# Kernel tuning notes

Hardware: AMD Instinct MI355X
Metric: run time of the kernel (lower is better)

## Reference

```python
import jax, jax.numpy as jnp
import numpy as np

HIDDEN = 2048
N_HEADS = 16
HEAD_DIM = HIDDEN // N_HEADS
ROPE_BASE = 10000.0


def rotate_half(x):
    half = x.shape[-1] // 2
    return jnp.concatenate((-x[..., half:], x[..., :half]), axis=-1)


def rope_cos_sin(seq_len, dtype):
    inv_freq = 1.0 / (ROPE_BASE ** (jnp.arange(0, HEAD_DIM, 2, dtype=jnp.float32) / HEAD_DIM))
    pos = jnp.arange(seq_len, dtype=jnp.float32)
    freqs = jnp.einsum('i,j->ij', pos, inv_freq)  # [S, hd/2]
    emb = jnp.concatenate((freqs, freqs), axis=-1)  # [S, hd]
    return jnp.cos(emb).astype(dtype), jnp.sin(emb).astype(dtype)


def setup_inputs() -> dict:
    key = jax.random.key(0)
    ks = jax.random.split(key, 9)
    B, S, H = 2, 2048, HIDDEN
    std = 1.0 / np.sqrt(H)
    return {
        'hidden_states': jax.random.normal(ks[0], (B, S, H), dtype=jnp.float32),
        'Wq': jax.random.uniform(ks[1], (H, H), jnp.float32, -std, std),
        'bq': jax.random.uniform(ks[2], (H,), jnp.float32, -std, std),
        'Wk': jax.random.uniform(ks[3], (H, H), jnp.float32, -std, std),
        'bk': jax.random.uniform(ks[4], (H,), jnp.float32, -std, std),
        'Wv': jax.random.uniform(ks[5], (H, H), jnp.float32, -std, std),
        'bv': jax.random.uniform(ks[6], (H,), jnp.float32, -std, std),
        'Wo': jax.random.uniform(ks[7], (H, H), jnp.float32, -std, std),
        'bo': jax.random.uniform(ks[8], (H,), jnp.float32, -std, std),
    }


def reference(hidden_states, Wq, bq, Wk, bk, Wv, bv, Wo, bo):
    B, S, H = hidden_states.shape
    scale = HEAD_DIM ** -0.5

    def proj(W, b):
        # torch Linear: x @ W.T + b
        y = jnp.einsum('bsh,oh->bso', hidden_states, W) + b
        return y.reshape(B, S, N_HEADS, HEAD_DIM).transpose(0, 2, 1, 3)  # [B,nh,S,hd]

    q = proj(Wq, bq)
    k = proj(Wk, bk)
    v = proj(Wv, bv)

    cos, sin = rope_cos_sin(S, hidden_states.dtype)  # [S, hd]
    cos = cos[None, None, :, :]
    sin = sin[None, None, :, :]
    q = q * cos + rotate_half(q) * sin
    k = k * cos + rotate_half(k) * sin

    scores = jnp.einsum('bhqd,bhkd->bhqk', q, k) * scale  # [B,nh,S,S]
    probs = jax.nn.softmax(scores, axis=-1)
    ctx = jnp.einsum('bhqk,bhkd->bhqd', probs, v)
    ctx = ctx.transpose(0, 2, 1, 3).reshape(B, S, H)
    return jnp.einsum('bsh,oh->bso', ctx, Wo) + bo
```

## Files before the change

kernel.cpp:

```cpp
#include <hip/hip_runtime.h>
#include <hip/hip_bf16.h>
#include <math.h>

#define HIDDEN 2048
#define NH 16
#define HD 128
#define NB 2
#define SEQ 2048
#define K_DIM 2048

typedef unsigned int u32;
typedef unsigned short ushort_t;
typedef __bf16 bf16x8 __attribute__((ext_vector_type(8)));
typedef float f32x4 __attribute__((ext_vector_type(4)));
typedef ushort_t u16x8 __attribute__((ext_vector_type(8)));

__device__ __forceinline__ void split1(float x, unsigned short& h, unsigned short& l) {
    u32 u = __float_as_uint(x);
    u32 hr = (u + 0x7FFFu + ((u >> 16) & 1u)) >> 16;
    h = (unsigned short)hr;
    float r = x - __uint_as_float(hr << 16);
    u32 u2 = __float_as_uint(r);
    l = (unsigned short)((u2 + 0x7FFFu + ((u2 >> 16) & 1u)) >> 16);
}

__device__ __forceinline__ ushort_t bf16r(float x) {
    u32 u = __float_as_uint(x);
    return (ushort_t)((u + 0x7FFFu + ((u >> 16) & 1u)) >> 16);
}

__device__ __forceinline__ void gl_lds16(const void* g, void* l) {
    __builtin_amdgcn_global_load_lds(
        (const __attribute__((address_space(1))) u32*)g,
        (__attribute__((address_space(3))) u32*)l, 16, 0, 0);
}

__global__ void k_rope_tables(float* __restrict__ ct, float* __restrict__ st) {
    int idx = blockIdx.x * 256 + threadIdx.x;
    int s = idx >> 6, d = idx & 63;
    double inv = pow(10000.0, -(double)d * (1.0 / 64.0));
    double ang = (double)s * inv;
    ct[idx] = (float)cos(ang);
    st[idx] = (float)sin(ang);
}

#define XG 2097152
#define WG 1048576
__global__ void k_cvt_all(const float4* __restrict__ X, const float4* __restrict__ W0,
                          const float4* __restrict__ W1, const float4* __restrict__ W2,
                          ushort4* __restrict__ Xh, ushort4* __restrict__ H0,
                          ushort4* __restrict__ H1, ushort4* __restrict__ H2) {
    int idx = blockIdx.x * 256 + threadIdx.x;
    const float4* src;
    ushort4* dst;
    int off;
    if (idx < XG) { src = X; dst = Xh; off = idx; }
    else {
        int t = idx - XG;
        int m = t >> 20;
        off = t & (WG - 1);
        src = (m == 0) ? W0 : (m == 1) ? W1 : W2;
        dst = (m == 0) ? H0 : (m == 1) ? H1 : H2;
    }
    float4 x = src[off];
    ushort4 h;
    h.x = bf16r(x.x); h.y = bf16r(x.y); h.z = bf16r(x.z); h.w = bf16r(x.w);
    dst[off] = h;
}

__global__ void k_split(const float4* __restrict__ src, ushort4* __restrict__ hi,
                        ushort4* __restrict__ lo) {
    int idx = blockIdx.x * 256 + threadIdx.x;
    float4 x = src[idx];
    ushort4 h, l;
    split1(x.x, h.x, l.x);
    split1(x.y, h.y, l.y);
    split1(x.z, h.z, l.z);
    split1(x.w, h.w, l.w);
    hi[idx] = h;
    lo[idx] = l;
}

#define BAR  __builtin_amdgcn_s_barrier()
#define VM8  asm volatile("s_waitcnt vmcnt(8)" ::: "memory")
#define VM0  asm volatile("s_waitcnt vmcnt(0)" ::: "memory")
#define PRIO1 __builtin_amdgcn_s_setprio(1)
#define PRIO0 __builtin_amdgcn_s_setprio(0)

#define STA(slot, half, kt) do { \
    const ushort_t* g_ = Xh + sgA + (size_t)((half) * 128) * 2048 + (size_t)(kt) * 64; \
    gl_lds16(g_, &As[slot][((half) * 128 + w * 16) * 64]); \
    gl_lds16(g_ + 8 * 2048, &As[slot][((half) * 128 + w * 16 + 8) * 64]); \
} while (0)

#define STB(slot, half, kt) do { \
    const ushort_t* g_ = Wsel + sgB + (size_t)((half) * 128) * 2048 + (size_t)(kt) * 64; \
    gl_lds16(g_, &Bs[slot][((half) * 128 + w * 16) * 64]); \
    gl_lds16(g_ + 8 * 2048, &Bs[slot][((half) * 128 + w * 16 + 8) * 64]); \
} while (0)

#define STAGE_T(slot, kt) do { \
    STA(slot, 0, kt); STA(slot, 1, kt); STB(slot, 0, kt); STB(slot, 1, kt); \
} while (0)

#define RD_A4(DST, slot, MB) \
    _Pragma("unroll") for (int mf = 0; mf < 4; mf++) { \
        DST[mf][0] = *(const bf16x8*)&As[slot][arow + ((MB) + mf) * 1024 + cc0]; \
        DST[mf][1] = *(const bf16x8*)&As[slot][arow + ((MB) + mf) * 1024 + cc1]; \
    }

#define RD_B2(DST, slot, NBB) \
    _Pragma("unroll") for (int nf = 0; nf < 2; nf++) { \
        DST[nf][0] = *(const bf16x8*)&Bs[slot][brow + ((NBB) + nf) * 1024 + cc0]; \
        DST[nf][1] = *(const bf16x8*)&Bs[slot][brow + ((NBB) + nf) * 1024 + cc1]; \
    }

#define PH_MFMA(AF, BF, MB, NBB) do { PRIO1; \
    _Pragma("unroll") for (int mf = 0; mf < 4; mf++) \
    _Pragma("unroll") for (int nf = 0; nf < 2; nf++) { \
        acc[(MB) + mf][(NBB) + nf] = __builtin_amdgcn_mfma_f32_16x16x32_bf16( \
            AF[mf][0], BF[nf][0], acc[(MB) + mf][(NBB) + nf], 0, 0, 0); \
        acc[(MB) + mf][(NBB) + nf] = __builtin_amdgcn_mfma_f32_16x16x32_bf16( \
            AF[mf][1], BF[nf][1], acc[(MB) + mf][(NBB) + nf], 0, 0, 0); \
    } PRIO0; } while (0)

#define KTILE(slot) do { \
    RD_A4(a03, slot, 0); RD_B2(b01, slot, 0); \
    RD_A4(a47, slot, 4); RD_B2(b23, slot, 2); \
    PH_MFMA(a03, b01, 0, 0); \
    PH_MFMA(a47, b01, 4, 0); \
    PH_MFMA(a03, b23, 0, 2); \
    PH_MFMA(a47, b23, 4, 2); \
} while (0)

__global__ __launch_bounds__(512, 2)
void k_gemm_qkv8(const ushort_t* __restrict__ Xh,
                 const ushort_t* __restrict__ W0, const ushort_t* __restrict__ W1,
                 const ushort_t* __restrict__ W2,
                 const float* __restrict__ b0, const float* __restrict__ b1,
                 const float* __restrict__ b2,
                 float* __restrict__ o0, float* __restrict__ o1, float* __restrict__ o2) {
    __shared__ ushort_t As[2][256 * 64];
    __shared__ ushort_t Bs[2][256 * 64];
    const int tid = threadIdx.x;
    const int lane = tid & 63;
    const int w = tid >> 6;
    const int wm = w >> 2;
    const int wn = w & 3;
    const int quad = lane >> 4;
    const int l15 = lane & 15;

    int bid = blockIdx.x;
    bid = (bid & 7) * 48 + (bid >> 3);
    const int bx = bid & 15;
    const int by = bid >> 4;
    const int m0 = bx << 8;
    const int mat = by >> 3;
    const int n0 = (by & 7) << 8;
    const ushort_t* Wsel = (mat == 0) ? W0 : (mat == 1) ? W1 : W2;
    const float* bias = (mat == 0) ? b0 : (mat == 1) ? b1 : b2;
    float* out = (mat == 0) ? o0 : (mat == 1) ? o1 : o2;

    const int lrow = lane >> 3;
    const int lcol8 = (((lane & 7) ^ lrow) << 3);
    const size_t sgA = (size_t)(m0 + w * 16 + lrow) * 2048 + lcol8;
    const size_t sgB = (size_t)(n0 + w * 16 + lrow) * 2048 + lcol8;

    const int arow = (wm * 128 + l15) * 64;
    const int brow = (wn * 64 + l15) * 64;
    const int cc0 = ((quad ^ (l15 & 7)) << 3);
    const int cc1 = cc0 ^ 32;

    f32x4 acc[8][4];
#pragma unroll
    for (int i = 0; i < 8; i++)
#pragma unroll
        for (int j = 0; j < 4; j++) acc[i][j] = (f32x4){0.f, 0.f, 0.f, 0.f};

    bf16x8 a03[4][2], a47[4][2], b01[2][2], b23[2][2];

    STAGE_T(0, 0);

    for (int it = 0; it < 16; ++it) {
        STAGE_T(1, 2 * it + 1);
        VM8;
        BAR;
        KTILE(0);
        BAR;
        if (it < 15) { STAGE_T(0, 2 * it + 2); VM8; } else { VM0; }
        BAR;
        KTILE(1);
        BAR;
    }

    float bcolv[4];
#pragma unroll
    for (int nf = 0; nf < 4; nf++) bcolv[nf] = bias[n0 + wn * 64 + nf * 16 + l15];

    const int mbase = m0 + wm * 128 + quad * 4;
#pragma unroll
    for (int mf = 0; mf < 8; mf++)
#pragma unroll
        for (int nf = 0; nf < 4; nf++) {
            const int n = n0 + wn * 64 + nf * 16 + l15;
            const int hh = n >> 7;
            const int d = n & 127;
#pragma unroll
            for (int r = 0; r < 4; r++) {
                const int m = mbase + mf * 16 + r;
                const int bb = m >> 11;
                const int s = m & (SEQ - 1);
                out[((size_t)(bb * NH + hh) * SEQ + s) * HD + d] = acc[mf][nf][r] + bcolv[nf];
            }
        }
}

__global__ __launch_bounds__(256)
void k_gemm_o(const ushort_t* __restrict__ Ah, const ushort_t* __restrict__ Al,
              const ushort_t* __restrict__ Bh, const ushort_t* __restrict__ Bl,
              const float* __restrict__ bias, float* __restrict__ out) {
    __shared__ ushort_t lds[4][128 * 32];
    const int tid = threadIdx.x;
    const int lane = tid & 63;
    const int w = tid >> 6;
    const int wm = w & 1, wn = w >> 1;
    const int quad = lane >> 4;
    const int l15 = lane & 15;
    const int m0 = blockIdx.x << 7;
    const int n0 = blockIdx.y << 7;
    const bool isA = (w < 2);

    const ushort_t* src = (w == 0) ? Ah : (w == 1) ? Al : (w == 2) ? Bh : Bl;
    const int lrow = lane >> 2;
    const int lk = (lane & 3) << 3;
    const ushort_t* gp[8];
    ushort_t* lp[8];
#pragma unroll
    for (int i = 0; i < 8; i++) {
        if (isA) {
            int m = m0 + i * 16 + lrow;
            int bb = m >> 11, s = m & (SEQ - 1);
            gp[i] = src + ((size_t)bb * NH * SEQ + s) * HD + lk;
        } else {
            gp[i] = src + (size_t)(n0 + i * 16 + lrow) * K_DIM + lk;
        }
        lp[i] = &lds[w][i * 512];
    }

    f32x4 acc[4][4];
#pragma unroll
    for (int i = 0; i < 4; i++)
#pragma unroll
        for (int j = 0; j < 4; j++) acc[i][j] = (f32x4){0.f, 0.f, 0.f, 0.f};

    const int aoff = (wm * 64 + l15) * 32 + quad * 8;
    const int boff = (wn * 64 + l15) * 32 + quad * 8;

#pragma unroll
    for (int i = 0; i < 8; i++) gl_lds16(gp[i], lp[i]);
    __syncthreads();
    bf16x8 ah[4], al[4], bh[4], bl[4];
#pragma unroll
    for (int f = 0; f < 4; f++) {
        ah[f] = *(const bf16x8*)&lds[0][aoff + f * 512];
        al[f] = *(const bf16x8*)&lds[1][aoff + f * 512];
        bh[f] = *(const bf16x8*)&lds[2][boff + f * 512];
        bl[f] = *(const bf16x8*)&lds[3][boff + f * 512];
    }

    for (int kt = 32; kt <= K_DIM; kt += 32) {
        __syncthreads();
        if (kt < K_DIM) {
            const size_t koff = isA ? ((size_t)(kt >> 7) * (SEQ * HD) + (kt & 127)) : (size_t)kt;
#pragma unroll
            for (int i = 0; i < 8; i++) gl_lds16(gp[i] + koff, lp[i]);
        }
#pragma unroll
        for (int fm = 0; fm < 4; fm++)
#pragma unroll
            for (int fn = 0; fn < 4; fn++) {
                acc[fm][fn] = __builtin_amdgcn_mfma_f32_16x16x32_bf16(ah[fm], bh[fn], acc[fm][fn], 0, 0, 0);
                acc[fm][fn] = __builtin_amdgcn_mfma_f32_16x16x32_bf16(ah[fm], bl[fn], acc[fm][fn], 0, 0, 0);
                acc[fm][fn] = __builtin_amdgcn_mfma_f32_16x16x32_bf16(al[fm], bh[fn], acc[fm][fn], 0, 0, 0);
            }
        if (kt < K_DIM) {
            __syncthreads();
#pragma unroll
            for (int f = 0; f < 4; f++) {
                ah[f] = *(const bf16x8*)&lds[0][aoff + f * 512];
                al[f] = *(const bf16x8*)&lds[1][aoff + f * 512];
                bh[f] = *(const bf16x8*)&lds[2][boff + f * 512];
                bl[f] = *(const bf16x8*)&lds[3][boff + f * 512];
            }
        }
    }

    float bcolv[4];
#pragma unroll
    for (int fn = 0; fn < 4; fn++) bcolv[fn] = bias[n0 + wn * 64 + fn * 16 + l15];

    const int mb = m0 + wm * 64 + quad * 4;
    const int nb = n0 + wn * 64 + l15;
#pragma unroll
    for (int fm = 0; fm < 4; fm++)
#pragma unroll
        for (int fn = 0; fn < 4; fn++)
#pragma unroll
            for (int r = 0; r < 4; r++)
                out[(size_t)(mb + fm * 16 + r) * HIDDEN + nb + fn * 16] =
                    acc[fm][fn][r] + bcolv[fn];
}

__global__ void k_rope_pack(const float* __restrict__ q, const float* __restrict__ k,
                            const float* __restrict__ ct, const float* __restrict__ st,
                            ushort_t* __restrict__ Qb, ushort_t* __restrict__ Kb) {
    int idx = blockIdx.x * 256 + threadIdx.x;
    int d = idx & 63;
    int s = (idx >> 6) & (SEQ - 1);
    int bh = idx >> 17;
    size_t base = ((size_t)bh * SEQ + s) * HD;
    float c = ct[(s << 6) + d], sn = st[(s << 6) + d];
    const float scq = 0.08838834764831845f;
    float q0 = q[base + d], q1 = q[base + d + 64];
    Qb[base + d]      = bf16r((q0 * c - q1 * sn) * scq);
    Qb[base + d + 64] = bf16r((q1 * c + q0 * sn) * scq);
    float k0 = k[base + d], k1 = k[base + d + 64];
    Kb[base + d]      = bf16r(k0 * c - k1 * sn);
    Kb[base + d + 64] = bf16r(k1 * c + k0 * sn);
}

__global__ __launch_bounds__(256)
void k_vpack(const float* __restrict__ v, ushort_t* __restrict__ vt) {
    __shared__ float t[64][65];
    const int tid = threadIdx.x;
    const int bh = blockIdx.z;
    const int s0 = blockIdx.x << 6;
    const int d0 = blockIdx.y << 6;
    const float* src = v + ((size_t)bh * SEQ + s0) * HD + d0;
    const int rr = tid >> 4;
    const int cc = (tid & 15) << 2;
#pragma unroll
    for (int i = 0; i < 4; i++) {
        float4 x = *(const float4*)(src + (size_t)(i * 16 + rr) * HD + cc);
        t[i * 16 + rr][cc] = x.x;
        t[i * 16 + rr][cc + 1] = x.y;
        t[i * 16 + rr][cc + 2] = x.z;
        t[i * 16 + rr][cc + 3] = x.w;
    }
    __syncthreads();
    const int dr = tid >> 2;
    const int sc_ = (tid & 3) << 4;
    ushort_t* dst = vt + ((size_t)bh * HD + d0 + dr) * SEQ + s0 + sc_;
    u16x8 o0, o1;
#pragma unroll
    for (int u = 0; u < 8; u++) o0[u] = bf16r(t[sc_ + u][dr]);
#pragma unroll
    for (int u = 0; u < 8; u++) o1[u] = bf16r(t[sc_ + 8 + u][dr]);
    *(u16x8*)dst = o0;
    *(u16x8*)(dst + 8) = o1;
}

__global__ __launch_bounds__(256, 2)
void k_flash_mfma(const ushort_t* __restrict__ Qb, const ushort_t* __restrict__ Kb,
                  const ushort_t* __restrict__ Vt,
                  ushort_t* __restrict__ ch, ushort_t* __restrict__ cl) {
    __shared__ ushort_t KV[128 * 136];
    __shared__ ushort_t Ps[128 * 136];
    const int tid = threadIdx.x;
    const int lane = tid & 63;
    const int w = tid >> 6;
    const int quad = lane >> 4;
    const int l15 = lane & 15;
    const int bi = blockIdx.x;
    const int bh = bi & 31;
    const int qt = bi >> 5;
    const ushort_t* Qg = Qb + ((size_t)bh * SEQ + ((size_t)qt << 7)) * HD;
    const ushort_t* Kg = Kb + (size_t)bh * SEQ * HD;
    const ushort_t* Vg = Vt + (size_t)bh * HD * SEQ;

    bf16x8 qf[2][4];
#pragma unroll
    for (int qi = 0; qi < 2; qi++)
#pragma unroll
        for (int ks = 0; ks < 4; ks++)
            qf[qi][ks] = *(const bf16x8*)(Qg + (size_t)(w * 32 + qi * 16 + l15) * HD + ks * 32 + quad * 8);

    const int sr = tid >> 4;
    const int sc8 = (tid & 15) << 3;

    u16x8 Kreg[8], Vreg[8];
#pragma unroll
    for (int i = 0; i < 8; i++)
        Kreg[i] = *(const u16x8*)(Kg + (size_t)(i * 16 + sr) * HD + sc8);
#pragma unroll
    for (int i = 0; i < 8; i++)
        Vreg[i] = *(const u16x8*)(Vg + (size_t)(i * 16 + sr) * SEQ + sc8);

    f32x4 acc[2][8];
#pragma unroll
    for (int qi = 0; qi < 2; qi++)
#pragma unroll
        for (int d = 0; d < 8; d++) acc[qi][d] = (f32x4){0.f, 0.f, 0.f, 0.f};
    float lp[2] = {0.f, 0.f};

    for (int kt = 0; kt < SEQ; kt += 128) {
        const int np = kt + 128;
        __syncthreads();
#pragma unroll
        for (int i = 0; i < 8; i++)
            *(u16x8*)&KV[(i * 16 + sr) * 136 + sc8] = Kreg[i];
        if (np < SEQ) {
#pragma unroll
            for (int i = 0; i < 8; i++)
                Kreg[i] = *(const u16x8*)(Kg + (size_t)(np + i * 16 + sr) * HD + sc8);
        }
        __syncthreads();

        f32x4 sc[2][8];
#pragma unroll
        for (int qi = 0; qi < 2; qi++)
#pragma unroll
            for (int j = 0; j < 8; j++) sc[qi][j] = (f32x4){0.f, 0.f, 0.f, 0.f};
#pragma unroll
        for (int ks = 0; ks < 4; ks++) {
#pragma unroll
            for (int jh = 0; jh < 2; jh++) {
                bf16x8 kf[4];
#pragma unroll
                for (int j = 0; j < 4; j++)
                    kf[j] = *(const bf16x8*)&KV[((jh * 4 + j) * 16 + l15) * 136 + ks * 32 + quad * 8];
#pragma unroll
                for (int qi = 0; qi < 2; qi++)
#pragma unroll
                    for (int j = 0; j < 4; j++)
                        sc[qi][jh * 4 + j] = __builtin_amdgcn_mfma_f32_16x16x32_bf16(
                            kf[j], qf[qi][ks], sc[qi][jh * 4 + j], 0, 0, 0);
            }
        }

#pragma unroll
        for (int qi = 0; qi < 2; qi++) {
            const int prow = (w * 32 + qi * 16 + l15) * 136 + quad * 4;
#pragma unroll
            for (int j = 0; j < 8; j++) {
                float p0 = __expf(sc[qi][j][0]);
                float p1 = __expf(sc[qi][j][1]);
                float p2 = __expf(sc[qi][j][2]);
                float p3 = __expf(sc[qi][j][3]);
                lp[qi] += (p0 + p1) + (p2 + p3);
                __hip_bfloat162 lo2 = __float22bfloat162_rn({p0, p1});
                __hip_bfloat162 hi2 = __float22bfloat162_rn({p2, p3});
                uint2 pk = make_uint2(*(u32*)&lo2, *(u32*)&hi2);
                *(uint2*)&Ps[prow + j * 16] = pk;
            }
        }
        __syncthreads();
#pragma unroll
        for (int i = 0; i < 8; i++)
            *(u16x8*)&KV[(i * 16 + sr) * 136 + sc8] = Vreg[i];
        if (np < SEQ) {
#pragma unroll
            for (int i = 0; i < 8; i++)
                Vreg[i] = *(const u16x8*)(Vg + (size_t)(i * 16 + sr) * SEQ + np + sc8);
        }
        __syncthreads();

#pragma unroll
        for (int ks = 0; ks < 4; ks++) {
            bf16x8 pf[2];
#pragma unroll
            for (int qi = 0; qi < 2; qi++)
                pf[qi] = *(const bf16x8*)&Ps[(w * 32 + qi * 16 + l15) * 136 + ks * 32 + quad * 8];
#pragma unroll
            for (int db = 0; db < 8; db++) {
                bf16x8 vf = *(const bf16x8*)&KV[(db * 16 + l15) * 136 + ks * 32 + quad * 8];
#pragma unroll
                for (int qi = 0; qi < 2; qi++)
                    acc[qi][db] = __builtin_amdgcn_mfma_f32_16x16x32_bf16(vf, pf[qi], acc[qi][db], 0, 0, 0);
            }
        }
    }

    float inv[2];
#pragma unroll
    for (int qi = 0; qi < 2; qi++) {
        float l = lp[qi];
        l += __shfl_xor(l, 16);
        l += __shfl_xor(l, 32);
        inv[qi] = 1.0f / l;
    }
    const size_t obase = ((size_t)bh * SEQ + ((size_t)qt << 7)) * HD;

    __syncthreads();
#pragma unroll
    for (int qi = 0; qi < 2; qi++)
#pragma unroll
        for (int db = 0; db < 8; db++) {
            ushort4 hh;
            ushort_t dum;
            split1(acc[qi][db][0] * inv[qi], hh.x, dum);
            split1(acc[qi][db][1] * inv[qi], hh.y, dum);
            split1(acc[qi][db][2] * inv[qi], hh.z, dum);
            split1(acc[qi][db][3] * inv[qi], hh.w, dum);
            *(ushort4*)&Ps[(w * 32 + qi * 16 + l15) * 136 + db * 16 + quad * 4] = hh;
        }
    __syncthreads();
#pragma unroll
    for (int t = 0; t < 8; t++) {
        int c = t * 256 + tid;
        int row = c >> 4, col8 = (c & 15) << 3;
        *(u16x8*)&ch[obase + (size_t)row * HD + col8] = *(const u16x8*)&Ps[row * 136 + col8];
    }
    __syncthreads();
#pragma unroll
    for (int qi = 0; qi < 2; qi++)
#pragma unroll
        for (int db = 0; db < 8; db++) {
            ushort4 ll;
            ushort_t dum;
            split1(acc[qi][db][0] * inv[qi], dum, ll.x);
            split1(acc[qi][db][1] * inv[qi], dum, ll.y);
            split1(acc[qi][db][2] * inv[qi], dum, ll.z);
            split1(acc[qi][db][3] * inv[qi], dum, ll.w);
            *(ushort4*)&Ps[(w * 32 + qi * 16 + l15) * 136 + db * 16 + quad * 4] = ll;
        }
    __syncthreads();
#pragma unroll
    for (int t = 0; t < 8; t++) {
        int c = t * 256 + tid;
        int row = c >> 4, col8 = (c & 15) << 3;
        *(u16x8*)&cl[obase + (size_t)row * HD + col8] = *(const u16x8*)&Ps[row * 136 + col8];
    }
}

extern "C" void kernel_launch(void* const* d_in, const int* in_sizes, int n_in,
                              void* d_out, int out_size, void* d_ws, size_t ws_size,
                              hipStream_t stream) {
    const float* X  = (const float*)d_in[0];
    const float* Wq = (const float*)d_in[1];
    const float* bq = (const float*)d_in[2];
    const float* Wk = (const float*)d_in[3];
    const float* bk = (const float*)d_in[4];
    const float* Wv = (const float*)d_in[5];
    const float* bv = (const float*)d_in[6];
    const float* Wo = (const float*)d_in[7];
    const float* bo = (const float*)d_in[8];
    float* out = (float*)d_out;

    const size_t QS = (size_t)NB * NH * SEQ * HD;
    const size_t WS = (size_t)HIDDEN * HIDDEN;
    float* q_ws = (float*)d_ws;
    float* k_ws = q_ws + QS;
    float* v_ws = k_ws + QS;
    float* cost = v_ws + QS;
    float* sint = cost + (size_t)SEQ * 64;
    ushort_t* Xh = (ushort_t*)(sint + (size_t)SEQ * 64);
    ushort_t* Wh0 = Xh + QS;
    ushort_t* Wh1 = Wh0 + WS;
    ushort_t* Wh2 = Wh1 + WS;
    ushort_t* Woh = Wh2 + WS;
    ushort_t* Wol = Woh + WS;
    ushort_t* Kb  = Wol + WS;
    ushort_t* Vtb = Kb + QS;
    ushort_t* ctxh = (ushort_t*)q_ws;
    ushort_t* ctxl = ctxh + QS;

    k_rope_tables<<<(SEQ * 64) / 256, 256, 0, stream>>>(cost, sint);

    k_cvt_all<<<(XG + 3 * WG) / 256, 256, 0, stream>>>(
        (const float4*)X, (const float4*)Wq, (const float4*)Wk, (const float4*)Wv,
        (ushort4*)Xh, (ushort4*)Wh0, (ushort4*)Wh1, (ushort4*)Wh2);
    k_split<<<WS / 4 / 256, 256, 0, stream>>>((const float4*)Wo, (ushort4*)Woh, (ushort4*)Wol);

    k_gemm_qkv8<<<384, 512, 0, stream>>>(Xh, Wh0, Wh1, Wh2, bq, bk, bv,
                                         q_ws, k_ws, v_ws);

    ushort_t* Qbb = Xh;
    k_rope_pack<<<(NB * NH * SEQ * 64) / 256, 256, 0, stream>>>(q_ws, k_ws, cost, sint, Qbb, Kb);
    k_vpack<<<dim3(SEQ / 64, HD / 64, NB * NH), 256, 0, stream>>>(v_ws, Vtb);

    k_flash_mfma<<<512, 256, 0, stream>>>(Qbb, Kb, Vtb, ctxh, ctxl);

    k_gemm_o<<<dim3(32, 16), 256, 0, stream>>>(ctxh, ctxl, Woh, Wol, bo, out);
}
```

Measured before the change: 495.4 us.

## Deepen software pipelining in QKV and output projection GEMMs

The QKV GEMM switches from double-buffered 64-wide K tiles to a four-slot ring of 32-wide K tiles. It prefetches two stages ahead and overlaps LDS fragment reads for the next tile with MFMAs on the current one. The output projection GEMM becomes a new 512-thread kernel with 256x128 tiles, a three-slot LDS ring, register double-buffered fragments and swizzled LDS layout, launched with a block-index remap for locality. This trades more barriers per K step and VM0 waits in the O GEMM for better latency hiding and larger per-block reuse.

```diff
diff --git a/kernel.cpp b/kernel.cpp
--- a/kernel.cpp
+++ b/kernel.cpp
@@ -82,56 +82,34 @@
 }
 
 #define BAR  __builtin_amdgcn_s_barrier()
-#define VM8  asm volatile("s_waitcnt vmcnt(8)" ::: "memory")
+#define VM6  asm volatile("s_waitcnt vmcnt(6)" ::: "memory")
+#define VM4  asm volatile("s_waitcnt vmcnt(4)" ::: "memory")
 #define VM0  asm volatile("s_waitcnt vmcnt(0)" ::: "memory")
 #define PRIO1 __builtin_amdgcn_s_setprio(1)
 #define PRIO0 __builtin_amdgcn_s_setprio(0)
 
-#define STA(slot, half, kt) do { \
-    const ushort_t* g_ = Xh + sgA + (size_t)((half) * 128) * 2048 + (size_t)(kt) * 64; \
-    gl_lds16(g_, &As[slot][((half) * 128 + w * 16) * 64]); \
-    gl_lds16(g_ + 8 * 2048, &As[slot][((half) * 128 + w * 16 + 8) * 64]); \
+#define QSTAGE(slot, kt) do { \
+    const ushort_t* gA_ = Xh + sgA + (size_t)(kt) * 32; \
+    gl_lds16(gA_, &As[slot][(w * 32) * 32]); \
+    gl_lds16(gA_ + 16 * 2048, &As[slot][(w * 32 + 16) * 32]); \
+    const ushort_t* gB_ = Wsel + sgB + (size_t)(kt) * 32; \
+    gl_lds16(gB_, &Bs[slot][(w * 32) * 32]); \
+    gl_lds16(gB_ + 16 * 2048, &Bs[slot][(w * 32 + 16) * 32]); \
 } while (0)
 
-#define STB(slot, half, kt) do { \
-    const ushort_t* g_ = Wsel + sgB + (size_t)((half) * 128) * 2048 + (size_t)(kt) * 64; \
-    gl_lds16(g_, &Bs[slot][((half) * 128 + w * 16) * 64]); \
-    gl_lds16(g_ + 8 * 2048, &Bs[slot][((half) * 128 + w * 16 + 8) * 64]); \
+#define QRD(AD, BD, slot) do { \
+    _Pragma("unroll") for (int mf = 0; mf < 8; mf++) \
+        AD[mf] = *(const bf16x8*)&As[slot][arow + mf * 512 + ccq]; \
+    _Pragma("unroll") for (int nf = 0; nf < 4; nf++) \
+        BD[nf] = *(const bf16x8*)&Bs[slot][brow + nf * 512 + ccq]; \
 } while (0)
 
-#define STAGE_T(slot, kt) do { \
-    STA(slot, 0, kt); STA(slot, 1, kt); STB(slot, 0, kt); STB(slot, 1, kt); \
-} while (0)
-
-#define RD_A4(DST, slot, MB) \
-    _Pragma("unroll") for (int mf = 0; mf < 4; mf++) { \
-        DST[mf][0] = *(const bf16x8*)&As[slot][arow + ((MB) + mf) * 1024 + cc0]; \
-        DST[mf][1] = *(const bf16x8*)&As[slot][arow + ((MB) + mf) * 1024 + cc1]; \
-    }
-
-#define RD_B2(DST, slot, NBB) \
-    _Pragma("unroll") for (int nf = 0; nf < 2; nf++) { \
-        DST[nf][0] = *(const bf16x8*)&Bs[slot][brow + ((NBB) + nf) * 1024 + cc0]; \
-        DST[nf][1] = *(const bf16x8*)&Bs[slot][brow + ((NBB) + nf) * 1024 + cc1]; \
-    }
-
-#define PH_MFMA(AF, BF, MB, NBB) do { PRIO1; \
-    _Pragma("unroll") for (int mf = 0; mf < 4; mf++) \
-    _Pragma("unroll") for (int nf = 0; nf < 2; nf++) { \
-        acc[(MB) + mf][(NBB) + nf] = __builtin_amdgcn_mfma_f32_16x16x32_bf16( \
-            AF[mf][0], BF[nf][0], acc[(MB) + mf][(NBB) + nf], 0, 0, 0); \
-        acc[(MB) + mf][(NBB) + nf] = __builtin_amdgcn_mfma_f32_16x16x32_bf16( \
-            AF[mf][1], BF[nf][1], acc[(MB) + mf][(NBB) + nf], 0, 0, 0); \
-    } PRIO0; } while (0)
-
-#define KTILE(slot) do { \
-    RD_A4(a03, slot, 0); RD_B2(b01, slot, 0); \
-    RD_A4(a47, slot, 4); RD_B2(b23, slot, 2); \
-    PH_MFMA(a03, b01, 0, 0); \
-    PH_MFMA(a47, b01, 4, 0); \
-    PH_MFMA(a03, b23, 0, 2); \
-    PH_MFMA(a47, b23, 4, 2); \
-} while (0)
+#define QMFMA(AD, BD) do { PRIO1; \
+    _Pragma("unroll") for (int mf = 0; mf < 8; mf++) \
+    _Pragma("unroll") for (int nf = 0; nf < 4; nf++) \
+        acc[mf][nf] = __builtin_amdgcn_mfma_f32_16x16x32_bf16( \
+            AD[mf], BD[nf], acc[mf][nf], 0, 0, 0); \
+    PRIO0; } while (0)
 
 __global__ __launch_bounds__(512, 2)
 void k_gemm_qkv8(const ushort_t* __restrict__ Xh,
@@ -140,8 +118,8 @@
                  const float* __restrict__ b0, const float* __restrict__ b1,
                  const float* __restrict__ b2,
                  float* __restrict__ o0, float* __restrict__ o1, float* __restrict__ o2) {
-    __shared__ ushort_t As[2][256 * 64];
-    __shared__ ushort_t Bs[2][256 * 64];
+    __shared__ ushort_t As[4][256 * 32];
+    __shared__ ushort_t Bs[4][256 * 32];
     const int tid = threadIdx.x;
     const int lane = tid & 63;
     const int w = tid >> 6;
@@ -161,15 +139,14 @@
     const float* bias = (mat == 0) ? b0 : (mat == 1) ? b1 : b2;
     float* out = (mat == 0) ? o0 : (mat == 1) ? o1 : o2;
 
-    const int lrow = lane >> 3;
-    const int lcol8 = (((lane & 7) ^ lrow) << 3);
-    const size_t sgA = (size_t)(m0 + w * 16 + lrow) * 2048 + lcol8;
-    const size_t sgB = (size_t)(n0 + w * 16 + lrow) * 2048 + lcol8;
-
-    const int arow = (wm * 128 + l15) * 64;
-    const int brow = (wn * 64 + l15) * 64;
-    const int cc0 = ((quad ^ (l15 & 7)) << 3);
-    const int cc1 = cc0 ^ 32;
+    const int lrow4 = lane >> 2;
+    const int col8 = (((lane & 3) ^ ((lrow4 >> 1) & 3)) << 3);
+    const size_t sgA = (size_t)(m0 + w * 32 + lrow4) * 2048 + col8;
+    const size_t sgB = (size_t)(n0 + w * 32 + lrow4) * 2048 + col8;
+
+    const int arow = (wm * 128 + l15) * 32;
+    const int brow = (wn * 64 + l15) * 32;
+    const int ccq = ((quad ^ ((l15 >> 1) & 3)) << 3);
 
     f32x4 acc[8][4];
 #pragma unroll
@@ -177,21 +154,22 @@
 #pragma unroll
         for (int j = 0; j < 4; j++) acc[i][j] = (f32x4){0.f, 0.f, 0.f, 0.f};
 
-    bf16x8 a03[4][2], a47[4][2], b01[2][2], b23[2][2];
-
-    STAGE_T(0, 0);
-
-    for (int it = 0; it < 16; ++it) {
-        STAGE_T(1, 2 * it + 1);
-        VM8;
-        BAR;
-        KTILE(0);
-        BAR;
-        if (it < 15) { STAGE_T(0, 2 * it + 2); VM8; } else { VM0; }
-        BAR;
-        KTILE(1);
-        BAR;
-    }
+    bf16x8 aA[8], bA[4], aB[8], bB[4];
+
+    QSTAGE(0, 0); QSTAGE(1, 1);
+    VM4; BAR;
+    QRD(aA, bA, 0);
+
+    for (int p = 0; p < 60; p += 4) {
+        QSTAGE(2, p + 2); VM4; BAR; QRD(aB, bB, 1); QMFMA(aA, bA);
+        QSTAGE(3, p + 3); VM4; BAR; QRD(aA, bA, 2); QMFMA(aB, bB);
+        QSTAGE(0, p + 4); VM4; BAR; QRD(aB, bB, 3); QMFMA(aA, bA);
+        QSTAGE(1, p + 5); VM4; BAR; QRD(aA, bA, 0); QMFMA(aB, bB);
+    }
+    QSTAGE(2, 62); VM4; BAR; QRD(aB, bB, 1); QMFMA(aA, bA);
+    QSTAGE(3, 63); VM4; BAR; QRD(aA, bA, 2); QMFMA(aB, bB);
+    VM0; BAR;                QRD(aB, bB, 3); QMFMA(aA, bA);
+    QMFMA(aB, bB);
 
     float bcolv[4];
 #pragma unroll
@@ -215,37 +193,68 @@
         }
 }
 
-__global__ __launch_bounds__(256)
-void k_gemm_o(const ushort_t* __restrict__ Ah, const ushort_t* __restrict__ Al,
-              const ushort_t* __restrict__ Bh, const ushort_t* __restrict__ Bl,
-              const float* __restrict__ bias, float* __restrict__ out) {
-    __shared__ ushort_t lds[4][128 * 32];
+#define OSTAGE(slot, kt) do { \
+    const size_t koA = (size_t)((kt) >> 2) * ((size_t)SEQ * HD) + (size_t)((kt) & 3) * 32; \
+    const size_t koB = (size_t)(kt) * 32; \
+    gl_lds16(Ah + sgA0 + koA, &Ah_s[slot][(w * 32) * 32]); \
+    gl_lds16(Ah + sgA0 + 16 * HD + koA, &Ah_s[slot][(w * 32 + 16) * 32]); \
+    gl_lds16(Al + sgA0 + koA, &Al_s[slot][(w * 32) * 32]); \
+    gl_lds16(Al + sgA0 + 16 * HD + koA, &Al_s[slot][(w * 32 + 16) * 32]); \
+    gl_lds16(Bh + sgB0 + koB, &Bh_s[slot][(w * 16) * 32]); \
+    gl_lds16(Bl + sgB0 + koB, &Bl_s[slot][(w * 16) * 32]); \
+} while (0)
+
+#define ORD(AH, AL, BH, BL, slot) do { \
+    _Pragma("unroll") for (int f = 0; f < 4; f++) { \
+        AH[f] = *(const bf16x8*)&Ah_s[slot][aro + f * 512 + cco]; \
+        AL[f] = *(const bf16x8*)&Al_s[slot][aro + f * 512 + cco]; \
+        BH[f] = *(const bf16x8*)&Bh_s[slot][bro + f * 512 + cco]; \
+        BL[f] = *(const bf16x8*)&Bl_s[slot][bro + f * 512 + cco]; \
+    } \
+} while (0)
+
+#define OMFMA(AH, AL, BH, BL) do { PRIO1; \
+    _Pragma("unroll") for (int mf = 0; mf < 4; mf++) \
+    _Pragma("unroll") for (int nf = 0; nf < 4; nf++) { \
+        acc[mf][nf] = __builtin_amdgcn_mfma_f32_16x16x32_bf16( \
+            AH[mf], BH[nf], acc[mf][nf], 0, 0, 0); \
+        acc[mf][nf] = __builtin_amdgcn_mfma_f32_16x16x32_bf16( \
+            AH[mf], BL[nf], acc[mf][nf], 0, 0, 0); \
+        acc[mf][nf] = __builtin_amdgcn_mfma_f32_16x16x32_bf16( \
+            AL[mf], BH[nf], acc[mf][nf], 0, 0, 0); \
+    } PRIO0; } while (0)
+
+__global__ __launch_bounds__(512, 2)
+void k_gemm_o2(const ushort_t* __restrict__ Ah, const ushort_t* __restrict__ Al,
+               const ushort_t* __restrict__ Bh, const ushort_t* __restrict__ Bl,
+               const float* __restrict__ bias, float* __restrict__ out) {
+    __shared__ ushort_t Ah_s[3][256 * 32];
+    __shared__ ushort_t Al_s[3][256 * 32];
+    __shared__ ushort_t Bh_s[3][128 * 32];
+    __shared__ ushort_t Bl_s[3][128 * 32];
     const int tid = threadIdx.x;
     const int lane = tid & 63;
     const int w = tid >> 6;
-    const int wm = w & 1, wn = w >> 1;
+    const int wm = w >> 1;
+    const int wn = w & 1;
     const int quad = lane >> 4;
     const int l15 = lane & 15;
-    const int m0 = blockIdx.x << 7;
-    const int n0 = blockIdx.y << 7;
-    const bool isA = (w < 2);
-
-    const ushort_t* src = (w == 0) ? Ah : (w == 1) ? Al : (w == 2) ? Bh : Bl;
-    const int lrow = lane >> 2;
-    const int lk = (lane & 3) << 3;
-    const ushort_t* gp[8];
-    ushort_t* lp[8];
-#pragma unroll
-    for (int i = 0; i < 8; i++) {
-        if (isA) {
-            int m = m0 + i * 16 + lrow;
-            int bb = m >> 11, s = m & (SEQ - 1);
-            gp[i] = src + ((size_t)bb * NH * SEQ + s) * HD + lk;
-        } else {
-            gp[i] = src + (size_t)(n0 + i * 16 + lrow) * K_DIM + lk;
-        }
-        lp[i] = &lds[w][i * 512];
-    }
+
+    int bid = blockIdx.x;
+    bid = (bid & 7) * 32 + (bid >> 3);
+    const int bx = bid & 15;
+    const int by = bid >> 4;
+    const int m0 = bx << 8;
+    const int n0 = by << 7;
+
+    const int lrow4 = lane >> 2;
+    const int col8 = (((lane & 3) ^ ((lrow4 >> 1) & 3)) << 3);
+    const size_t sgA0 = ((size_t)(m0 >> 11) * NH * SEQ + (size_t)((m0 & (SEQ - 1)) + w * 32 + lrow4)) * HD + col8;
+    const size_t sgB0 = (size_t)(n0 + w * 16 + lrow4) * K_DIM + col8;
+
+    const int aro = (wm * 64 + l15) * 32;
+    const int bro = (wn * 64 + l15) * 32;
+    const int cco = ((quad ^ ((l15 >> 1) & 3)) << 3);
 
     f32x4 acc[4][4];
 #pragma unroll
@@ -253,51 +262,31 @@
 #pragma unroll
         for (int j = 0; j < 4; j++) acc[i][j] = (f32x4){0.f, 0.f, 0.f, 0.f};
 
-    const int aoff = (wm * 64 + l15) * 32 + quad * 8;
-    const int boff = (wn * 64 + l15) * 32 + quad * 8;
-
-#pragma unroll
-    for (int i = 0; i < 8; i++) gl_lds16(gp[i], lp[i]);
-    __syncthreads();
-    bf16x8 ah[4], al[4], bh[4], bl[4];
-#pragma unroll
-    for (int f = 0; f < 4; f++) {
-        ah[f] = *(const bf16x8*)&lds[0][aoff + f * 512];
-        al[f] = *(const bf16x8*)&lds[1][aoff + f * 512];
-        bh[f] = *(const bf16x8*)&lds[2][boff + f * 512];
-        bl[f] = *(const bf16x8*)&lds[3][boff + f * 512];
-    }
-
-    for (int kt = 32; kt <= K_DIM; kt += 32) {
-        __syncthreads();
-        if (kt < K_DIM) {
-            const size_t koff = isA ? ((size_t)(kt >> 7) * (SEQ * HD) + (kt & 127)) : (size_t)kt;
-#pragma unroll
-            for (int i = 0; i < 8; i++) gl_lds16(gp[i] + koff, lp[i]);
-        }
-#pragma unroll
-        for (int fm = 0; fm < 4; fm++)
-#pragma unroll
-            for (int fn = 0; fn < 4; fn++) {
-                acc[fm][fn] = __builtin_amdgcn_mfma_f32_16x16x32_bf16(ah[fm], bh[fn], acc[fm][fn], 0, 0, 0);
-                acc[fm][fn] = __builtin_amdgcn_mfma_f32_16x16x32_bf16(ah[fm], bl[fn], acc[fm][fn], 0, 0, 0);
-                acc[fm][fn] = __builtin_amdgcn_mfma_f32_16x16x32_bf16(al[fm], bh[fn], acc[fm][fn], 0, 0, 0);
-            }
-        if (kt < K_DIM) {
-            __syncthreads();
-#pragma unroll
-            for (int f = 0; f < 4; f++) {
-                ah[f] = *(const bf16x8*)&lds[0][aoff + f * 512];
-                al[f] = *(const bf16x8*)&lds[1][aoff + f * 512];
-                bh[f] = *(const bf16x8*)&lds[2][boff + f * 512];
-                bl[f] = *(const bf16x8*)&lds[3][boff + f * 512];
-            }
-        }
-    }
+    bf16x8 ahA[4], alA[4], bhA[4], blA[4];
+    bf16x8 ahB[4], alB[4], bhB[4], blB[4];
+
+    OSTAGE(0, 0);
+    OSTAGE(1, 1);
+    VM6; BAR;
+    ORD(ahA, alA, bhA, blA, 0);
+
+    for (int it = 0; it < 10; ++it) {
+        const int q = 6 * it;
+        VM0; BAR; OSTAGE(2, q + 2); ORD(ahB, alB, bhB, blB, 1); OMFMA(ahA, alA, bhA, blA);
+        VM0; BAR; OSTAGE(0, q + 3); ORD(ahA, alA, bhA, blA, 2); OMFMA(ahB, alB, bhB, blB);
+        VM0; BAR; OSTAGE(1, q + 4); ORD(ahB, alB, bhB, blB, 0); OMFMA(ahA, alA, bhA, blA);
+        VM0; BAR; OSTAGE(2, q + 5); ORD(ahA, alA, bhA, blA, 1); OMFMA(ahB, alB, bhB, blB);
+        VM0; BAR; OSTAGE(0, q + 6); ORD(ahB, alB, bhB, blB, 2); OMFMA(ahA, alA, bhA, blA);
+        VM0; BAR; OSTAGE(1, q + 7); ORD(ahA, alA, bhA, blA, 0); OMFMA(ahB, alB, bhB, blB);
+    }
+    VM0; BAR; OSTAGE(2, 62); ORD(ahB, alB, bhB, blB, 1); OMFMA(ahA, alA, bhA, blA);
+    VM0; BAR; OSTAGE(0, 63); ORD(ahA, alA, bhA, blA, 2); OMFMA(ahB, alB, bhB, blB);
+    VM0; BAR;                ORD(ahB, alB, bhB, blB, 0); OMFMA(ahA, alA, bhA, blA);
+    OMFMA(ahB, alB, bhB, blB);
 
     float bcolv[4];
 #pragma unroll
-    for (int fn = 0; fn < 4; fn++) bcolv[fn] = bias[n0 + wn * 64 + fn * 16 + l15];
+    for (int nf = 0; nf < 4; nf++) bcolv[nf] = bias[n0 + wn * 64 + nf * 16 + l15];
 
     const int mb = m0 + wm * 64 + quad * 4;
     const int nb = n0 + wn * 64 + l15;
@@ -581,5 +570,5 @@
 
     k_flash_mfma<<<512, 256, 0, stream>>>(Qbb, Kb, Vtb, ctxh, ctxl);
 
-    k_gemm_o<<<dim3(32, 16), 256, 0, stream>>>(ctxh, ctxl, Woh, Wol, bo, out);
-}
+    k_gemm_o2<<<256, 512, 0, stream>>>(ctxh, ctxl, Woh, Wol, bo, out);
+}
```

Measured after the change: 513.8 us. 1.04x slower.
